# Performance work log

Hardware: AMD Instinct MI355X
Metric: run time of the kernel (lower is better)

The kernel has to match this reference:

```python
import jax, jax.numpy as jnp
import numpy as np

N = 50000      # node_num
C = 64         # num_classes
G = 3          # number of metapath graphs (len(g))
E = 1200000    # edges per metapath graph
L = 2          # layers (PLPConv propagation steps)
D = 256        # input feature dim (feat_dims[0])
H = 256        # hidden_dim


def setup_inputs() -> dict:
    key = jax.random.key(0)
    ks = jax.random.split(key, 13)
    features0 = jax.random.normal(ks[0], (N, D), jnp.float32)
    labels = jax.random.randint(ks[1], (N,), 0, C)
    labels_one_hot = jax.nn.one_hot(labels, C, dtype=jnp.float32)
    # label_init: soft labels, rows on the simplex
    label_init = jax.nn.softmax(jax.random.normal(ks[2], (N, C), jnp.float32), axis=-1)
    train_mask = (jax.random.uniform(ks[3], (N, 1)) < 0.5).astype(jnp.float32)
    src = jax.random.randint(ks[4], (G, E), 0, N, dtype=jnp.int32)
    dst = jax.random.randint(ks[5], (G, E), 0, N, dtype=jnp.int32)
    # per-layer, per-graph learned edge logits (xavier-ish small init)
    e_edges = 0.1 * jax.random.normal(ks[6], (L, G, E), jnp.float32)
    attention = 0.5 * jax.random.normal(ks[7], (N, G), jnp.float32)
    alpha = 0.5 * jax.random.normal(ks[8], (N, 1), jnp.float32)
    W1 = jax.random.normal(ks[9], (D, H), jnp.float32) / np.sqrt(D)
    b1 = jnp.zeros((H,), jnp.float32)
    W2 = jax.random.normal(ks[10], (H, C), jnp.float32) / np.sqrt(H)
    b2 = jnp.zeros((C,), jnp.float32)
    return {"features0": features0, "label_init": label_init,
            "labels_one_hot": labels_one_hot, "train_mask": train_mask,
            "src": src, "dst": dst, "e_edges": e_edges,
            "attention": attention, "alpha": alpha,
            "W1": W1, "b1": b1, "W2": W2, "b2": b2}


def _edge_softmax(e, dst, n):
    # softmax of per-edge scalar over incoming edges of each dst node
    m = jax.ops.segment_max(e, dst, num_segments=n)
    a = jnp.exp(e - m[dst])
    s = jax.ops.segment_sum(a, dst, num_segments=n)
    return a / s[dst]


def reference(features0, label_init, labels_one_hot, train_mask,
              src, dst, e_edges, attention, alpha, W1, b1, W2, b2):
    n = label_init.shape[0]
    masked_label = 1.0 - train_mask            # (~masked).float(), [N,1]
    masked_oh = labels_one_hot * train_mask    # labels_one_hot * masked, [N,C]

    # Label propagation over each metapath graph (PLPConv stack, activation=None)
    h_prime = []
    for i in range(G):
        h = label_init
        for l in range(L):
            a = _edge_softmax(e_edges[l, i], dst[i], n)         # [E]
            msg = h[src[i]] * a[:, None]                        # gather-mul [E,C]
            h = jax.ops.segment_sum(msg, dst[i], num_segments=n)  # scatter-sum [N,C]
            h = h * masked_label + masked_oh                    # clamp train labels
        h_prime.append(h)
    x = jnp.stack(h_prime, axis=-1)                             # [N,C,G]

    att_mp = jax.nn.softmax(attention, axis=1)                  # [N,G]
    logits_lp = jnp.einsum('ncg,ng->nc', x, att_mp)             # [N,C]

    # MLP2 (2 layers, dropout=0): relu(x W1 + b1) W2 + b2
    hm = jax.nn.relu(features0 @ W1 + b1)
    logits_ns = hm @ W2 + b2                                    # [N,C]

    logits = jax.nn.sigmoid(alpha) * logits_lp + jax.nn.sigmoid(-alpha) * logits_ns
    return (logits, logits_lp, logits_ns)
```

## Files before the change

### kernel.cpp

```cpp
#include <hip/hip_runtime.h>
#include <hip/hip_bf16.h>

#define NN 50000
#define CC 64
#define GG 3
#define EE 1200000
#define LL 2
#define DD 256
#define HH 256
#define NB 196
#define NBLK 293
#define NBK (GG * NB)
#define BKCAP 8192
#define CH 16384
#define CBLK 74


__device__ __forceinline__ ushort f2bf(float f) {
    unsigned b = __float_as_uint(f);
    return (ushort)((b + 0x7fffu + ((b >> 16) & 1u)) >> 16);
}
__device__ __forceinline__ float bf2f(unsigned u) {
    return __uint_as_float(u << 16);
}

typedef __attribute__((ext_vector_type(8))) short s8v;
typedef __attribute__((ext_vector_type(4))) float f4v;

template<int NWM, int NWN, bool A_FP32, bool OUT_RELU_BF16>
__global__ __launch_bounds__(256) void mfma_gemm_kernel(
    const void* __restrict__ Av, const ushort* __restrict__ Bt,
    const float* __restrict__ bias, void* __restrict__ Cv, int M, int Nc)
{
    static_assert(NWM * NWN == 4, "4 waves per block");
    const int tid = threadIdx.x;
    const int w = tid >> 6;
    const int l = tid & 63;
    const int wm = w / NWN;
    const int wn = w % NWN;
    const int r0 = blockIdx.x * (NWM * 64) + wm * 64;
    const int c0 = blockIdx.y * (NWN * 64) + wn * 64;
    const int lrow = l & 15;
    const int lk = (l >> 4) << 3;

    f4v acc[4][4] = {};

    for (int k0 = 0; k0 < 256; k0 += 32) {
        s8v a[4], b[4];
        #pragma unroll
        for (int i = 0; i < 4; i++) {
            int row = r0 + lrow + 16 * i;
            row = (row < M) ? row : (M - 1);
            if constexpr (A_FP32) {
                const float* Af = (const float*)Av;
                const float4* p = (const float4*)(Af + (size_t)row * 256 + k0 + lk);
                float4 f0 = p[0], f1 = p[1];
                union { ushort u[8]; s8v v; } t;
                t.u[0] = f2bf(f0.x); t.u[1] = f2bf(f0.y);
                t.u[2] = f2bf(f0.z); t.u[3] = f2bf(f0.w);
                t.u[4] = f2bf(f1.x); t.u[5] = f2bf(f1.y);
                t.u[6] = f2bf(f1.z); t.u[7] = f2bf(f1.w);
                a[i] = t.v;
            } else {
                const ushort* Ab = (const ushort*)Av;
                a[i] = *(const s8v*)(Ab + (size_t)row * 256 + k0 + lk);
            }
        }
        #pragma unroll
        for (int j = 0; j < 4; j++) {
            int col = c0 + lrow + 16 * j;
            b[j] = *(const s8v*)(Bt + (size_t)col * 256 + k0 + lk);
        }
        #pragma unroll
        for (int i = 0; i < 4; i++)
            #pragma unroll
            for (int j = 0; j < 4; j++)
                acc[i][j] = __builtin_amdgcn_mfma_f32_16x16x32_bf16(
                    a[i], b[j], acc[i][j], 0, 0, 0);
    }

    #pragma unroll
    for (int i = 0; i < 4; i++) {
        #pragma unroll
        for (int r = 0; r < 4; r++) {
            int row = r0 + 16 * i + (l >> 4) * 4 + r;
            if (row >= M) continue;
            #pragma unroll
            for (int j = 0; j < 4; j++) {
                int col = c0 + 16 * j + lrow;
                float v = acc[i][j][r] + bias[col];
                if constexpr (OUT_RELU_BF16) {
                    v = fmaxf(v, 0.f);
                    ((ushort*)Cv)[(size_t)row * Nc + col] = f2bf(v);
                } else {
                    ((float*)Cv)[(size_t)row * Nc + col] = v;
                }
            }
        }
    }
}

__global__ void wcvt_kernel(const float* __restrict__ W1,
                            const float* __restrict__ W2,
                            ushort* __restrict__ Wt1, ushort* __restrict__ Wt2)
{
    int idx = blockIdx.x * 256 + threadIdx.x;
    if (idx < 256 * 256) {
        int n = idx >> 8, k = idx & 255;
        Wt1[idx] = f2bf(W1[k * 256 + n]);
    } else {
        int i = idx - 256 * 256;
        if (i < 64 * 256) {
            int n = i >> 8, k = i & 255;
            Wt2[i] = f2bf(W2[k * 64 + n]);
        }
    }
}

__global__ void cvt_kernel(const float* __restrict__ in, ushort* __restrict__ out, int n4)
{
    int i = blockIdx.x * blockDim.x + threadIdx.x;
    if (i >= n4) return;
    float4 f = ((const float4*)in)[i];
    ushort4 u;
    u.x = f2bf(f.x); u.y = f2bf(f.y); u.z = f2bf(f.z); u.w = f2bf(f.w);
    ((ushort4*)out)[i] = u;
}

__global__ __launch_bounds__(256) void bhist_kernel(
    const int* __restrict__ dst, int* __restrict__ bcnt)
{
    int blk = blockIdx.x;
    int g = blk / NBLK;
    int bi = blk - g * NBLK;
    int base = bi * 4096;
    __shared__ int cnt[NB];
    int t = threadIdx.x;
    if (t < NB) cnt[t] = 0;
    __syncthreads();
    #pragma unroll
    for (int k = 0; k < 16; k++) {
        int e = base + k * 256 + t;
        if (e < EE) atomicAdd(&cnt[dst[g * EE + e] >> 8], 1);
    }
    __syncthreads();
    if (t < NB && cnt[t] > 0) atomicAdd(&bcnt[g * NB + t], cnt[t]);
}

__global__ void scan_bucket(const int* __restrict__ bcnt, int* __restrict__ bs)
{
    __shared__ int sd[256];
    __shared__ int s_run;
    int t = threadIdx.x;
    if (t == 0) s_run = 0;
    __syncthreads();
    for (int base = 0; base < NBK; base += 256) {
        int i = base + t;
        int v = (i < NBK) ? bcnt[i] : 0;
        sd[t] = v;
        __syncthreads();
        for (int o = 1; o < 256; o <<= 1) {
            int x = (t >= o) ? sd[t - o] : 0;
            __syncthreads();
            sd[t] += x;
            __syncthreads();
        }
        int run = s_run;
        __syncthreads();
        if (i < NBK) bs[i] = run + sd[t] - v;
        if (t == 255) s_run = run + sd[255];
        __syncthreads();
    }
    if (t == 0) bs[NBK] = GG * EE;
}

__global__ __launch_bounds__(1024) void binA_kernel(
    const int* __restrict__ dst, const int* __restrict__ src,
    const float* __restrict__ e_edges, const int* __restrict__ bucket_start,
    int* __restrict__ fill, uint2* __restrict__ staging)
{
    int blk = blockIdx.x;
    int g = blk / CBLK;
    int bi = blk - g * CBLK;
    int base = bi * CH;
    __shared__ uint2 rec[CH];
    __shared__ int cnt[NB];
    __shared__ int lstart[NB];
    __shared__ int cur[NB];
    __shared__ int gbase[NB];
    __shared__ int sd[256];
    int t = threadIdx.x;
    if (t < NB) cnt[t] = 0;
    __syncthreads();

    int myd[16];
    #pragma unroll
    for (int k = 0; k < 16; k++) {
        int e = base + k * 1024 + t;
        int d = (e < EE) ? dst[g * EE + e] : -1;
        myd[k] = d;
        if (d >= 0) atomicAdd(&cnt[d >> 8], 1);
    }
    __syncthreads();

    if (t < 256) sd[t] = (t < NB) ? cnt[t] : 0;
    __syncthreads();
    for (int o = 1; o < 256; o <<= 1) {
        int x = (t < 256 && t >= o) ? sd[t - o] : 0;
        __syncthreads();
        if (t < 256) sd[t] += x;
        __syncthreads();
    }
    if (t < NB) {
        int c = cnt[t];
        int ls = sd[t] - c;
        lstart[t] = ls;
        cur[t] = ls;
        int fo = (c > 0) ? atomicAdd(&fill[g * NB + t], c) : 0;
        gbase[t] = bucket_start[g * NB + t] + fo;
    }
    __syncthreads();

    #pragma unroll
    for (int k = 0; k < 16; k++) {
        int d = myd[k];
        if (d >= 0) {
            int e = base + k * 1024 + t;
            int pos = atomicAdd(&cur[d >> 8], 1);
            int idxg = g * EE + e;
            uint2 r;
            r.x = ((unsigned)f2bf(e_edges[idxg]) << 16) |
                  (unsigned)f2bf(e_edges[(size_t)(GG + g) * EE + e]);
            r.y = ((unsigned)src[idxg] << 16) | (unsigned)(d & 255);
            rec[pos] = r;
        }
    }
    __syncthreads();

    int w = t >> 6, lane = t & 63;
    for (int b = w; b < NB; b += 16) {
        int c = cnt[b];
        int ls = lstart[b];
        uint2* dp = staging + gbase[b];
        for (int i = lane; i < c; i += 64) dp[i] = rec[ls + i];
    }
}

__global__ __launch_bounds__(1024) void bucket_kernel(
    const uint2* __restrict__ staging, const int* __restrict__ bucket_start,
    int* __restrict__ row_start, unsigned* __restrict__ packed0,
    unsigned* __restrict__ packed1)
{
    int blk = blockIdx.x;
    int g = blk / NB;
    int bucket = blk - g * NB;
    int bn = bucket << 8;
    int bnodes = min(256, NN - bn);
    int sbase = bucket_start[blk];
    int n = bucket_start[blk + 1] - sbase;
    int segStart = sbase - g * EE;
    const uint2* st = staging + sbase;

    __shared__ int hist[256];
    __shared__ int sd[256];
    __shared__ int cur[256];
    __shared__ float sm[512];
    __shared__ ushort ab0[BKCAP];
    __shared__ ushort ab1[BKCAP];
    __shared__ ushort sb[BKCAP];
    int t = threadIdx.x;
    if (t < 256) hist[t] = 0;
    if (t < 512) sm[t] = 0.f;
    __syncthreads();

    for (int i = t; i < n; i += 1024) {
        uint2 r = st[i];
        int dl = r.y & 0xff;
        atomicAdd(&hist[dl], 1);
        atomicAdd(&sm[dl], __expf(bf2f(r.x >> 16)));
        atomicAdd(&sm[256 + dl], __expf(bf2f(r.x & 0xffffu)));
    }
    __syncthreads();

    if (t < 256) sd[t] = hist[t];
    __syncthreads();
    for (int o = 1; o < 256; o <<= 1) {
        int x = (t < 256 && t >= o) ? sd[t - o] : 0;
        __syncthreads();
        if (t < 256) sd[t] += x;
        __syncthreads();
    }
    if (t < 256) {
        cur[t] = sd[t] - hist[t];
        if (t < bnodes)
            row_start[(size_t)g * (NN + 1) + bn + t] = segStart + sd[t] - hist[t];
        if (hist[t] > 0) {
            sm[t] = 1.f / sm[t];
            sm[256 + t] = 1.f / sm[256 + t];
        }
    }
    if (bucket == NB - 1 && t == 0) row_start[(size_t)g * (NN + 1) + NN] = EE;
    __syncthreads();

    for (int i = t; i < n; i += 1024) {
        uint2 r = st[i];
        int dl = r.y & 0xff;
        int pos = atomicAdd(&cur[dl], 1);
        ab0[pos] = f2bf(__expf(bf2f(r.x >> 16)) * sm[dl]);
        ab1[pos] = f2bf(__expf(bf2f(r.x & 0xffffu)) * sm[256 + dl]);
        sb[pos] = (ushort)(r.y >> 16);
    }
    __syncthreads();

    for (int i = t; i < n; i += 1024) {
        unsigned s = sb[i];
        packed0[(size_t)sbase + i] = ((unsigned)ab0[i] << 16) | s;
        packed1[(size_t)sbase + i] = ((unsigned)ab1[i] << 16) | s;
    }
}

__device__ __forceinline__ void consume8(unsigned packed, int cnt,
                                         const ushort* __restrict__ tab,
                                         int lane, float& acc)
{
    for (int k0 = 0; k0 < cnt; k0 += 8) {
        unsigned pk[8];
        #pragma unroll
        for (int u = 0; u < 8; u++) pk[u] = __shfl(packed, k0 + u);
        float vals[8];
        #pragma unroll
        for (int u = 0; u < 8; u++)
            vals[u] = bf2f((unsigned)tab[(size_t)(pk[u] & 0xffffu) * 64 + lane]);
        #pragma unroll
        for (int u = 0; u < 8; u++)
            acc = fmaf(vals[u], __uint_as_float(pk[u] & 0xffff0000u), acc);
    }
}

__global__ __launch_bounds__(256) void prop0_kernel(
    const ushort* __restrict__ lab_bf, const float* __restrict__ labels_oh,
    const float* __restrict__ train_mask, const int* __restrict__ row_start,
    const unsigned* __restrict__ packed0, ushort* __restrict__ h_buf)
{
    int wid = (blockIdx.x * blockDim.x + threadIdx.x) >> 6;
    int lane = threadIdx.x & 63;
    if (wid >= GG * NN) return;
    int g = wid / NN;
    int v = wid - g * NN;
    const int* rs = row_start + (size_t)g * (NN + 1);
    int s = rs[v], tE = rs[v + 1];
    const unsigned* pk = packed0 + (size_t)g * EE;

    float acc = 0.f;
    for (int base = s; base < tE; base += 64) {
        int j = base + lane;
        unsigned packed = (j < tE) ? pk[j] : 0u;
        int cnt = min(64, tE - base);
        consume8(packed, cnt, lab_bf, lane, acc);
    }
    float tm = train_mask[v];
    float res = acc * (1.f - tm) + labels_oh[(size_t)v * 64 + lane] * tm;
    h_buf[(size_t)wid * 64 + lane] = f2bf(res);
}

__global__ __launch_bounds__(256) void final_kernel(
    const ushort* __restrict__ h_buf, const float* __restrict__ labels_oh,
    const float* __restrict__ train_mask, const float* __restrict__ attention,
    const float* __restrict__ alpha, const int* __restrict__ row_start,
    const unsigned* __restrict__ packed1, const float* __restrict__ out_ns,
    float* __restrict__ out_logits, float* __restrict__ out_lp)
{
    int wid = (blockIdx.x * blockDim.x + threadIdx.x) >> 6;
    int lane = threadIdx.x & 63;
    if (wid >= NN) return;
    int v = wid;
    float tm = train_mask[v];
    float ml = 1.f - tm;
    float moh = labels_oh[(size_t)v * 64 + lane] * tm;
    float a0 = attention[v * 3], a1 = attention[v * 3 + 1], a2 = attention[v * 3 + 2];
    float mxa = fmaxf(a0, fmaxf(a1, a2));
    float e0 = __expf(a0 - mxa), e1 = __expf(a1 - mxa), e2 = __expf(a2 - mxa);
    float ainv = 1.f / (e0 + e1 + e2);
    float attw[3] = {e0 * ainv, e1 * ainv, e2 * ainv};
    float lp = 0.f;
    #pragma unroll
    for (int g = 0; g < GG; g++) {
        const int* rs = row_start + (size_t)g * (NN + 1);
        int s = rs[v], tE = rs[v + 1];
        const unsigned* pk = packed1 + (size_t)g * EE;
        const ushort* hin = h_buf + (size_t)g * NN * 64;

        float acc = 0.f;
        for (int base = s; base < tE; base += 64) {
            int j = base + lane;
            unsigned packed = (j < tE) ? pk[j] : 0u;
            int cnt = min(64, tE - base);
            consume8(packed, cnt, hin, lane, acc);
        }
        float hf = acc * ml + moh;
        lp += attw[g] * hf;
    }
    size_t o = (size_t)v * 64 + lane;
    out_lp[o] = lp;
    float al = alpha[v];
    float sg = 1.f / (1.f + __expf(-al));
    out_logits[o] = sg * lp + (1.f - sg) * out_ns[o];
}

extern "C" void kernel_launch(void* const* d_in, const int* in_sizes, int n_in,
                              void* d_out, int out_size, void* d_ws, size_t ws_size,
                              hipStream_t stream)
{
    const float* features0  = (const float*)d_in[0];
    const float* label_init = (const float*)d_in[1];
    const float* labels_oh  = (const float*)d_in[2];
    const float* train_mask = (const float*)d_in[3];
    const int*   src        = (const int*)d_in[4];
    const int*   dst        = (const int*)d_in[5];
    const float* e_edges    = (const float*)d_in[6];
    const float* attention  = (const float*)d_in[7];
    const float* alpha      = (const float*)d_in[8];
    const float* W1         = (const float*)d_in[9];
    const float* b1         = (const float*)d_in[10];
    const float* W2         = (const float*)d_in[11];
    const float* b2         = (const float*)d_in[12];

    float* out        = (float*)d_out;
    float* out_logits = out;
    float* out_lp     = out + (size_t)NN * CC;
    float* out_ns     = out + 2 * (size_t)NN * CC;

    char* base = (char*)d_ws;
    size_t off = 0;
    auto alloc = [&](size_t bytes) -> void* {
        void* p = base + off;
        off = (off + bytes + 255) & ~(size_t)255;
        return p;
    };
    int*      bcnt         = (int*)alloc((size_t)NBK * sizeof(int));
    int*      fill         = (int*)alloc((size_t)NBK * sizeof(int));
    size_t    zero_bytes   = off;
    int*      bucket_start = (int*)alloc((size_t)(NBK + 1) * sizeof(int));
    int*      row_start    = (int*)alloc((size_t)GG * (NN + 1) * sizeof(int));
    uint2*    staging      = (uint2*)alloc((size_t)GG * EE * sizeof(uint2));
    unsigned* packed0      = (unsigned*)alloc((size_t)GG * EE * sizeof(unsigned));
    unsigned* packed1      = (unsigned*)alloc((size_t)GG * EE * sizeof(unsigned));
    ushort*   h_buf        = (ushort*)alloc((size_t)GG * NN * CC * sizeof(ushort));
    ushort*   lab_bf       = (ushort*)alloc((size_t)NN * CC * sizeof(ushort));

    ushort* Wt1   = (ushort*)packed0;
    ushort* Wt2   = Wt1 + 256 * 256;
    ushort* hm_bf = (ushort*)staging;

    wcvt_kernel<<<(256 * 256 + 64 * 256) / 256, 256, 0, stream>>>(W1, W2, Wt1, Wt2);
    mfma_gemm_kernel<2, 2, true, true><<<dim3((NN + 127) / 128, 2), 256, 0, stream>>>(
        features0, Wt1, b1, hm_bf, NN, HH);
    mfma_gemm_kernel<4, 1, false, false><<<dim3((NN + 255) / 256, 1), 256, 0, stream>>>(
        hm_bf, Wt2, b2, out_ns, NN, CC);

    cvt_kernel<<<(NN * CC / 4 + 255) / 256, 256, 0, stream>>>(
        label_init, lab_bf, NN * CC / 4);

    hipMemsetAsync(bcnt, 0, zero_bytes, stream);
    bhist_kernel<<<GG * NBLK, 256, 0, stream>>>(dst, bcnt);
    scan_bucket<<<1, 256, 0, stream>>>(bcnt, bucket_start);
    binA_kernel<<<GG * CBLK, 1024, 0, stream>>>(
        dst, src, e_edges, bucket_start, fill, staging);
    bucket_kernel<<<GG * NB, 1024, 0, stream>>>(
        staging, bucket_start, row_start, packed0, packed1);

    prop0_kernel<<<((size_t)GG * NN * 64 + 255) / 256, 256, 0, stream>>>(
        lab_bf, labels_oh, train_mask, row_start, packed0, h_buf);

    final_kernel<<<((size_t)NN * 64 + 255) / 256, 256, 0, stream>>>(
        h_buf, labels_oh, train_mask, attention, alpha, row_start, packed1,
        out_ns, out_logits, out_lp);
}
```

Before: 482.9 us.

## Split label tables into 32-channel planes and gather 8 edges per wave instruction

```diff
diff --git a/kernel.cpp b/kernel.cpp
--- a/kernel.cpp
+++ b/kernel.cpp
@@ -117,14 +117,37 @@
     }
 }
 
-__global__ void cvt_kernel(const float* __restrict__ in, ushort* __restrict__ out, int n4)
-{
-    int i = blockIdx.x * blockDim.x + threadIdx.x;
-    if (i >= n4) return;
-    float4 f = ((const float4*)in)[i];
-    ushort4 u;
-    u.x = f2bf(f.x); u.y = f2bf(f.y); u.z = f2bf(f.z); u.w = f2bf(f.w);
-    ((ushort4*)out)[i] = u;
+__global__ __launch_bounds__(256) void prep_kernel(
+    const float* __restrict__ label_init, const float* __restrict__ labels_oh,
+    const float* __restrict__ train_mask, ushort* __restrict__ lab_bf,
+    short* __restrict__ mid)
+{
+    int b = blockIdx.x;
+    if (b < 3125) {
+        int i = b * 256 + threadIdx.x;
+        int v = i >> 4;
+        int c4 = (i & 15) * 4;
+        float4 f = ((const float4*)label_init)[i];
+        ushort4 u;
+        u.x = f2bf(f.x); u.y = f2bf(f.y); u.z = f2bf(f.z); u.w = f2bf(f.w);
+        int pl = c4 >> 5;
+        *(ushort4*)(lab_bf + (size_t)pl * NN * 32 + (size_t)v * 32 + (c4 & 31)) = u;
+    } else {
+        int t = threadIdx.x;
+        int v = (b - 3125) * 16 + (t >> 4);
+        int sl = t & 15;
+        if (v < NN) {
+            float4 f = ((const float4*)(labels_oh + (size_t)v * 64))[sl];
+            float p = (float)(sl * 4);
+            float s = f.x * p + f.y * (p + 1.f) + f.z * (p + 2.f) + f.w * (p + 3.f);
+            s += __shfl_xor(s, 1); s += __shfl_xor(s, 2);
+            s += __shfl_xor(s, 4); s += __shfl_xor(s, 8);
+            if (sl == 0) {
+                float tm = train_mask[v];
+                mid[v] = (tm > 0.5f) ? (short)(s + 0.5f) : (short)-1;
+            }
+        }
+    }
 }
 
 __global__ __launch_bounds__(256) void bhist_kernel(
@@ -319,28 +342,32 @@
     }
 }
 
-__device__ __forceinline__ void consume8(unsigned packed, int cnt,
-                                         const ushort* __restrict__ tab,
-                                         int lane, float& acc)
-{
-    for (int k0 = 0; k0 < cnt; k0 += 8) {
-        unsigned pk[8];
-        #pragma unroll
-        for (int u = 0; u < 8; u++) pk[u] = __shfl(packed, k0 + u);
-        float vals[8];
-        #pragma unroll
-        for (int u = 0; u < 8; u++)
-            vals[u] = bf2f((unsigned)tab[(size_t)(pk[u] & 0xffffu) * 64 + lane]);
-        #pragma unroll
-        for (int u = 0; u < 8; u++)
-            acc = fmaf(vals[u], __uint_as_float(pk[u] & 0xffff0000u), acc);
+__device__ __forceinline__ void tile_pass(unsigned packed, int cnt,
+        const ushort* __restrict__ plane, unsigned loff, int sub, float acc[4])
+{
+    for (int q0 = 0; q0 < cnt; q0 += 32) {
+        uint2 gv[4]; float w[4];
+        #pragma unroll
+        for (int u = 0; u < 4; u++) {
+            unsigned pkq = __shfl(packed, q0 + 8 * u + sub);
+            w[u] = __uint_as_float(pkq & 0xffff0000u);
+            gv[u] = *(const uint2*)((const char*)plane +
+                                    (((pkq & 0xffffu) << 6) | loff));
+        }
+        #pragma unroll
+        for (int u = 0; u < 4; u++) {
+            acc[0] = fmaf(__uint_as_float(gv[u].x << 16),          w[u], acc[0]);
+            acc[1] = fmaf(__uint_as_float(gv[u].x & 0xffff0000u),  w[u], acc[1]);
+            acc[2] = fmaf(__uint_as_float(gv[u].y << 16),          w[u], acc[2]);
+            acc[3] = fmaf(__uint_as_float(gv[u].y & 0xffff0000u),  w[u], acc[3]);
+        }
     }
 }
 
 __global__ __launch_bounds__(256) void prop0_kernel(
-    const ushort* __restrict__ lab_bf, const float* __restrict__ labels_oh,
-    const float* __restrict__ train_mask, const int* __restrict__ row_start,
-    const unsigned* __restrict__ packed0, ushort* __restrict__ h_buf)
+    const ushort* __restrict__ lab_bf, const short* __restrict__ mid,
+    const int* __restrict__ row_start, const unsigned* __restrict__ packed0,
+    ushort* __restrict__ h_buf)
 {
     int wid = (blockIdx.x * blockDim.x + threadIdx.x) >> 6;
     int lane = threadIdx.x & 63;
@@ -350,61 +377,130 @@
     const int* rs = row_start + (size_t)g * (NN + 1);
     int s = rs[v], tE = rs[v + 1];
     const unsigned* pk = packed0 + (size_t)g * EE;
-
-    float acc = 0.f;
+    const ushort* pl0 = lab_bf;
+    const ushort* pl1 = lab_bf + (size_t)NN * 32;
+
+    unsigned loff = (lane & 7) << 3;
+    int sub = lane >> 3;
+    float a0[4] = {}, a1[4] = {};
     for (int base = s; base < tE; base += 64) {
         int j = base + lane;
         unsigned packed = (j < tE) ? pk[j] : 0u;
         int cnt = min(64, tE - base);
-        consume8(packed, cnt, lab_bf, lane, acc);
-    }
-    float tm = train_mask[v];
-    float res = acc * (1.f - tm) + labels_oh[(size_t)v * 64 + lane] * tm;
-    h_buf[(size_t)wid * 64 + lane] = f2bf(res);
+        tile_pass(packed, cnt, pl0, loff, sub, a0);
+        tile_pass(packed, cnt, pl1, loff, sub, a1);
+    }
+    #pragma unroll
+    for (int c = 0; c < 4; c++) {
+        a0[c] += __shfl_xor(a0[c], 8);
+        a0[c] += __shfl_xor(a0[c], 16);
+        a0[c] += __shfl_xor(a0[c], 32);
+        a1[c] += __shfl_xor(a1[c], 8);
+        a1[c] += __shfl_xor(a1[c], 16);
+        a1[c] += __shfl_xor(a1[c], 32);
+    }
+    int m = mid[v];
+    float ml = (m < 0) ? 1.f : 0.f;
+    ushort* hg = h_buf + (size_t)g * NN * 64;
+    int cb = (lane & 7) * 4;
+    if (lane < 8) {
+        ushort4 o;
+        o.x = f2bf(a0[0] * ml + ((cb + 0 == m) ? 1.f : 0.f));
+        o.y = f2bf(a0[1] * ml + ((cb + 1 == m) ? 1.f : 0.f));
+        o.z = f2bf(a0[2] * ml + ((cb + 2 == m) ? 1.f : 0.f));
+        o.w = f2bf(a0[3] * ml + ((cb + 3 == m) ? 1.f : 0.f));
+        *(ushort4*)(hg + (size_t)v * 32 + cb) = o;
+    } else if (lane < 16) {
+        int cc = cb + 32;
+        ushort4 o;
+        o.x = f2bf(a1[0] * ml + ((cc + 0 == m) ? 1.f : 0.f));
+        o.y = f2bf(a1[1] * ml + ((cc + 1 == m) ? 1.f : 0.f));
+        o.z = f2bf(a1[2] * ml + ((cc + 2 == m) ? 1.f : 0.f));
+        o.w = f2bf(a1[3] * ml + ((cc + 3 == m) ? 1.f : 0.f));
+        *(ushort4*)(hg + (size_t)NN * 32 + (size_t)v * 32 + cb) = o;
+    }
 }
 
 __global__ __launch_bounds__(256) void final_kernel(
-    const ushort* __restrict__ h_buf, const float* __restrict__ labels_oh,
-    const float* __restrict__ train_mask, const float* __restrict__ attention,
-    const float* __restrict__ alpha, const int* __restrict__ row_start,
-    const unsigned* __restrict__ packed1, const float* __restrict__ out_ns,
-    float* __restrict__ out_logits, float* __restrict__ out_lp)
+    const ushort* __restrict__ h_buf, const short* __restrict__ mid,
+    const float* __restrict__ attention, const float* __restrict__ alpha,
+    const int* __restrict__ row_start, const unsigned* __restrict__ packed1,
+    const float* __restrict__ out_ns, float* __restrict__ out_logits,
+    float* __restrict__ out_lp)
 {
     int wid = (blockIdx.x * blockDim.x + threadIdx.x) >> 6;
     int lane = threadIdx.x & 63;
     if (wid >= NN) return;
     int v = wid;
-    float tm = train_mask[v];
-    float ml = 1.f - tm;
-    float moh = labels_oh[(size_t)v * 64 + lane] * tm;
-    float a0 = attention[v * 3], a1 = attention[v * 3 + 1], a2 = attention[v * 3 + 2];
-    float mxa = fmaxf(a0, fmaxf(a1, a2));
-    float e0 = __expf(a0 - mxa), e1 = __expf(a1 - mxa), e2 = __expf(a2 - mxa);
+    float t0 = attention[v * 3], t1 = attention[v * 3 + 1], t2 = attention[v * 3 + 2];
+    float mxa = fmaxf(t0, fmaxf(t1, t2));
+    float e0 = __expf(t0 - mxa), e1 = __expf(t1 - mxa), e2 = __expf(t2 - mxa);
     float ainv = 1.f / (e0 + e1 + e2);
     float attw[3] = {e0 * ainv, e1 * ainv, e2 * ainv};
-    float lp = 0.f;
+
+    unsigned loff = (lane & 7) << 3;
+    int sub = lane >> 3;
+    float w0[4] = {}, w1[4] = {};
     #pragma unroll
     for (int g = 0; g < GG; g++) {
         const int* rs = row_start + (size_t)g * (NN + 1);
         int s = rs[v], tE = rs[v + 1];
         const unsigned* pk = packed1 + (size_t)g * EE;
-        const ushort* hin = h_buf + (size_t)g * NN * 64;
-
-        float acc = 0.f;
+        const ushort* hp0 = h_buf + (size_t)g * NN * 64;
+        const ushort* hp1 = hp0 + (size_t)NN * 32;
+        float b0[4] = {}, b1[4] = {};
         for (int base = s; base < tE; base += 64) {
             int j = base + lane;
             unsigned packed = (j < tE) ? pk[j] : 0u;
             int cnt = min(64, tE - base);
-            consume8(packed, cnt, hin, lane, acc);
-        }
-        float hf = acc * ml + moh;
-        lp += attw[g] * hf;
-    }
-    size_t o = (size_t)v * 64 + lane;
-    out_lp[o] = lp;
-    float al = alpha[v];
-    float sg = 1.f / (1.f + __expf(-al));
-    out_logits[o] = sg * lp + (1.f - sg) * out_ns[o];
+            tile_pass(packed, cnt, hp0, loff, sub, b0);
+            tile_pass(packed, cnt, hp1, loff, sub, b1);
+        }
+        float aw = attw[g];
+        #pragma unroll
+        for (int c = 0; c < 4; c++) {
+            w0[c] = fmaf(aw, b0[c], w0[c]);
+            w1[c] = fmaf(aw, b1[c], w1[c]);
+        }
+    }
+    #pragma unroll
+    for (int c = 0; c < 4; c++) {
+        w0[c] += __shfl_xor(w0[c], 8);
+        w0[c] += __shfl_xor(w0[c], 16);
+        w0[c] += __shfl_xor(w0[c], 32);
+        w1[c] += __shfl_xor(w1[c], 8);
+        w1[c] += __shfl_xor(w1[c], 16);
+        w1[c] += __shfl_xor(w1[c], 32);
+    }
+    int m = mid[v];
+    float ml = (m < 0) ? 1.f : 0.f;
+    if (lane < 16) {
+        int pl = lane >> 3;
+        int cb = (lane & 7) * 4 + pl * 32;
+        float4 lpv;
+        if (pl == 0) {
+            lpv.x = w0[0] * ml + ((cb + 0 == m) ? 1.f : 0.f);
+            lpv.y = w0[1] * ml + ((cb + 1 == m) ? 1.f : 0.f);
+            lpv.z = w0[2] * ml + ((cb + 2 == m) ? 1.f : 0.f);
+            lpv.w = w0[3] * ml + ((cb + 3 == m) ? 1.f : 0.f);
+        } else {
+            lpv.x = w1[0] * ml + ((cb + 0 == m) ? 1.f : 0.f);
+            lpv.y = w1[1] * ml + ((cb + 1 == m) ? 1.f : 0.f);
+            lpv.z = w1[2] * ml + ((cb + 2 == m) ? 1.f : 0.f);
+            lpv.w = w1[3] * ml + ((cb + 3 == m) ? 1.f : 0.f);
+        }
+        size_t o = (size_t)v * 64 + cb;
+        *(float4*)(out_lp + o) = lpv;
+        float al = alpha[v];
+        float sg = 1.f / (1.f + __expf(-al));
+        float4 ns = *(const float4*)(out_ns + o);
+        float4 lg;
+        lg.x = sg * lpv.x + (1.f - sg) * ns.x;
+        lg.y = sg * lpv.y + (1.f - sg) * ns.y;
+        lg.z = sg * lpv.z + (1.f - sg) * ns.z;
+        lg.w = sg * lpv.w + (1.f - sg) * ns.w;
+        *(float4*)(out_logits + o) = lg;
+    }
 }
 
 extern "C" void kernel_launch(void* const* d_in, const int* in_sizes, int n_in,
@@ -447,6 +543,7 @@
     unsigned* packed1      = (unsigned*)alloc((size_t)GG * EE * sizeof(unsigned));
     ushort*   h_buf        = (ushort*)alloc((size_t)GG * NN * CC * sizeof(ushort));
     ushort*   lab_bf       = (ushort*)alloc((size_t)NN * CC * sizeof(ushort));
+    short*    mid          = (short*)alloc((size_t)NN * sizeof(short));
 
     ushort* Wt1   = (ushort*)packed0;
     ushort* Wt2   = Wt1 + 256 * 256;
@@ -458,8 +555,8 @@
     mfma_gemm_kernel<4, 1, false, false><<<dim3((NN + 255) / 256, 1), 256, 0, stream>>>(
         hm_bf, Wt2, b2, out_ns, NN, CC);
 
-    cvt_kernel<<<(NN * CC / 4 + 255) / 256, 256, 0, stream>>>(
-        label_init, lab_bf, NN * CC / 4);
+    prep_kernel<<<6250, 256, 0, stream>>>(label_init, labels_oh, train_mask,
+                                          lab_bf, mid);
 
     hipMemsetAsync(bcnt, 0, zero_bytes, stream);
     bhist_kernel<<<GG * NBLK, 256, 0, stream>>>(dst, bcnt);
@@ -470,9 +567,9 @@
         staging, bucket_start, row_start, packed0, packed1);
 
     prop0_kernel<<<((size_t)GG * NN * 64 + 255) / 256, 256, 0, stream>>>(
-        lab_bf, labels_oh, train_mask, row_start, packed0, h_buf);
+        lab_bf, mid, row_start, packed0, h_buf);
 
     final_kernel<<<((size_t)NN * 64 + 255) / 256, 256, 0, stream>>>(
-        h_buf, labels_oh, train_mask, attention, alpha, row_start, packed1,
+        h_buf, mid, attention, alpha, row_start, packed1,
         out_ns, out_logits, out_lp);
 }
```

Measured after the change: 512.3 us. +6.1%, slower.

## Drop destination histogram pass using fixed-capacity bucket staging and merge prep kernels

Applied to the files above, without the earlier changes.

```diff
diff --git a/kernel.cpp b/kernel.cpp
--- a/kernel.cpp
+++ b/kernel.cpp
@@ -9,7 +9,6 @@
 #define DD 256
 #define HH 256
 #define NB 196
-#define NBLK 293
 #define NBK (GG * NB)
 #define BKCAP 8192
 #define CH 16384
@@ -100,54 +99,34 @@
     }
 }
 
-__global__ void wcvt_kernel(const float* __restrict__ W1,
-                            const float* __restrict__ W2,
-                            ushort* __restrict__ Wt1, ushort* __restrict__ Wt2)
-{
-    int idx = blockIdx.x * 256 + threadIdx.x;
-    if (idx < 256 * 256) {
-        int n = idx >> 8, k = idx & 255;
-        Wt1[idx] = f2bf(W1[k * 256 + n]);
+__global__ __launch_bounds__(256) void prep_kernel(
+    const float* __restrict__ label_init,
+    const float* __restrict__ W1, const float* __restrict__ W2,
+    ushort* __restrict__ lab_bf, ushort* __restrict__ Wt1,
+    ushort* __restrict__ Wt2)
+{
+    int b = blockIdx.x;
+    int t = threadIdx.x;
+    if (b < 3125) {
+        int i = b * 256 + t;
+        float4 f = ((const float4*)label_init)[i];
+        ushort4 u;
+        u.x = f2bf(f.x); u.y = f2bf(f.y); u.z = f2bf(f.z); u.w = f2bf(f.w);
+        ((ushort4*)lab_bf)[i] = u;
     } else {
-        int i = idx - 256 * 256;
-        if (i < 64 * 256) {
+        int idx = (b - 3125) * 256 + t;
+        if (idx < 256 * 256) {
+            int n = idx >> 8, k = idx & 255;
+            Wt1[idx] = f2bf(W1[k * 256 + n]);
+        } else {
+            int i = idx - 256 * 256;
             int n = i >> 8, k = i & 255;
             Wt2[i] = f2bf(W2[k * 64 + n]);
         }
     }
 }
 
-__global__ void cvt_kernel(const float* __restrict__ in, ushort* __restrict__ out, int n4)
-{
-    int i = blockIdx.x * blockDim.x + threadIdx.x;
-    if (i >= n4) return;
-    float4 f = ((const float4*)in)[i];
-    ushort4 u;
-    u.x = f2bf(f.x); u.y = f2bf(f.y); u.z = f2bf(f.z); u.w = f2bf(f.w);
-    ((ushort4*)out)[i] = u;
-}
-
-__global__ __launch_bounds__(256) void bhist_kernel(
-    const int* __restrict__ dst, int* __restrict__ bcnt)
-{
-    int blk = blockIdx.x;
-    int g = blk / NBLK;
-    int bi = blk - g * NBLK;
-    int base = bi * 4096;
-    __shared__ int cnt[NB];
-    int t = threadIdx.x;
-    if (t < NB) cnt[t] = 0;
-    __syncthreads();
-    #pragma unroll
-    for (int k = 0; k < 16; k++) {
-        int e = base + k * 256 + t;
-        if (e < EE) atomicAdd(&cnt[dst[g * EE + e] >> 8], 1);
-    }
-    __syncthreads();
-    if (t < NB && cnt[t] > 0) atomicAdd(&bcnt[g * NB + t], cnt[t]);
-}
-
-__global__ void scan_bucket(const int* __restrict__ bcnt, int* __restrict__ bs)
+__global__ void scan_bucket(const int* __restrict__ fill, int* __restrict__ bs)
 {
     __shared__ int sd[256];
     __shared__ int s_run;
@@ -156,7 +135,7 @@
     __syncthreads();
     for (int base = 0; base < NBK; base += 256) {
         int i = base + t;
-        int v = (i < NBK) ? bcnt[i] : 0;
+        int v = (i < NBK) ? fill[i] : 0;
         sd[t] = v;
         __syncthreads();
         for (int o = 1; o < 256; o <<= 1) {
@@ -176,8 +155,8 @@
 
 __global__ __launch_bounds__(1024) void binA_kernel(
     const int* __restrict__ dst, const int* __restrict__ src,
-    const float* __restrict__ e_edges, const int* __restrict__ bucket_start,
-    int* __restrict__ fill, uint2* __restrict__ staging)
+    const float* __restrict__ e_edges, int* __restrict__ fill,
+    uint2* __restrict__ staging)
 {
     int blk = blockIdx.x;
     int g = blk / CBLK;
@@ -217,7 +196,7 @@
         lstart[t] = ls;
         cur[t] = ls;
         int fo = (c > 0) ? atomicAdd(&fill[g * NB + t], c) : 0;
-        gbase[t] = bucket_start[g * NB + t] + fo;
+        gbase[t] = (g * NB + t) * BKCAP + fo;
     }
     __syncthreads();
 
@@ -241,25 +220,25 @@
     for (int b = w; b < NB; b += 16) {
         int c = cnt[b];
         int ls = lstart[b];
-        uint2* dp = staging + gbase[b];
+        uint2* dp = staging + (size_t)gbase[b];
         for (int i = lane; i < c; i += 64) dp[i] = rec[ls + i];
     }
 }
 
 __global__ __launch_bounds__(1024) void bucket_kernel(
-    const uint2* __restrict__ staging, const int* __restrict__ bucket_start,
-    int* __restrict__ row_start, unsigned* __restrict__ packed0,
-    unsigned* __restrict__ packed1)
+    const uint2* __restrict__ staging, const int* __restrict__ fill,
+    const int* __restrict__ out_start, int* __restrict__ row_start,
+    unsigned* __restrict__ packed0, unsigned* __restrict__ packed1)
 {
     int blk = blockIdx.x;
     int g = blk / NB;
     int bucket = blk - g * NB;
     int bn = bucket << 8;
     int bnodes = min(256, NN - bn);
-    int sbase = bucket_start[blk];
-    int n = bucket_start[blk + 1] - sbase;
-    int segStart = sbase - g * EE;
-    const uint2* st = staging + sbase;
+    int n = fill[blk];
+    int obase = out_start[blk];
+    int segStart = obase - g * EE;
+    const uint2* st = staging + (size_t)blk * BKCAP;
 
     __shared__ int hist[256];
     __shared__ int sd[256];
@@ -314,8 +293,8 @@
 
     for (int i = t; i < n; i += 1024) {
         unsigned s = sb[i];
-        packed0[(size_t)sbase + i] = ((unsigned)ab0[i] << 16) | s;
-        packed1[(size_t)sbase + i] = ((unsigned)ab1[i] << 16) | s;
+        packed0[(size_t)obase + i] = ((unsigned)ab0[i] << 16) | s;
+        packed1[(size_t)obase + i] = ((unsigned)ab1[i] << 16) | s;
     }
 }
 
@@ -354,7 +333,7 @@
     float acc = 0.f;
     for (int base = s; base < tE; base += 64) {
         int j = base + lane;
-        unsigned packed = (j < tE) ? pk[j] : 0u;
+        unsigned packed = (j < tE) ? __builtin_nontemporal_load(pk + j) : 0u;
         int cnt = min(64, tE - base);
         consume8(packed, cnt, lab_bf, lane, acc);
     }
@@ -393,7 +372,7 @@
         float acc = 0.f;
         for (int base = s; base < tE; base += 64) {
             int j = base + lane;
-            unsigned packed = (j < tE) ? pk[j] : 0u;
+            unsigned packed = (j < tE) ? __builtin_nontemporal_load(pk + j) : 0u;
             int cnt = min(64, tE - base);
             consume8(packed, cnt, hin, lane, acc);
         }
@@ -437,37 +416,32 @@
         off = (off + bytes + 255) & ~(size_t)255;
         return p;
     };
-    int*      bcnt         = (int*)alloc((size_t)NBK * sizeof(int));
     int*      fill         = (int*)alloc((size_t)NBK * sizeof(int));
     size_t    zero_bytes   = off;
-    int*      bucket_start = (int*)alloc((size_t)(NBK + 1) * sizeof(int));
+    int*      out_start    = (int*)alloc((size_t)(NBK + 1) * sizeof(int));
     int*      row_start    = (int*)alloc((size_t)GG * (NN + 1) * sizeof(int));
-    uint2*    staging      = (uint2*)alloc((size_t)GG * EE * sizeof(uint2));
+    uint2*    staging      = (uint2*)alloc((size_t)NBK * BKCAP * sizeof(uint2));
     unsigned* packed0      = (unsigned*)alloc((size_t)GG * EE * sizeof(unsigned));
     unsigned* packed1      = (unsigned*)alloc((size_t)GG * EE * sizeof(unsigned));
     ushort*   h_buf        = (ushort*)alloc((size_t)GG * NN * CC * sizeof(ushort));
     ushort*   lab_bf       = (ushort*)alloc((size_t)NN * CC * sizeof(ushort));
 
-    ushort* Wt1   = (ushort*)packed0;
-    ushort* Wt2   = Wt1 + 256 * 256;
-    ushort* hm_bf = (ushort*)staging;
-
-    wcvt_kernel<<<(256 * 256 + 64 * 256) / 256, 256, 0, stream>>>(W1, W2, Wt1, Wt2);
+    ushort* Wt1     = (ushort*)packed0;
+    ushort* Wt2     = Wt1 + 256 * 256;
+    ushort* hm_bf   = (ushort*)staging;
+
+    hipMemsetAsync(fill, 0, zero_bytes, stream);
+    prep_kernel<<<3445, 256, 0, stream>>>(label_init, W1, W2, lab_bf, Wt1, Wt2);
+
     mfma_gemm_kernel<2, 2, true, true><<<dim3((NN + 127) / 128, 2), 256, 0, stream>>>(
         features0, Wt1, b1, hm_bf, NN, HH);
     mfma_gemm_kernel<4, 1, false, false><<<dim3((NN + 255) / 256, 1), 256, 0, stream>>>(
         hm_bf, Wt2, b2, out_ns, NN, CC);
 
-    cvt_kernel<<<(NN * CC / 4 + 255) / 256, 256, 0, stream>>>(
-        label_init, lab_bf, NN * CC / 4);
-
-    hipMemsetAsync(bcnt, 0, zero_bytes, stream);
-    bhist_kernel<<<GG * NBLK, 256, 0, stream>>>(dst, bcnt);
-    scan_bucket<<<1, 256, 0, stream>>>(bcnt, bucket_start);
-    binA_kernel<<<GG * CBLK, 1024, 0, stream>>>(
-        dst, src, e_edges, bucket_start, fill, staging);
+    binA_kernel<<<GG * CBLK, 1024, 0, stream>>>(dst, src, e_edges, fill, staging);
+    scan_bucket<<<1, 256, 0, stream>>>(fill, out_start);
     bucket_kernel<<<GG * NB, 1024, 0, stream>>>(
-        staging, bucket_start, row_start, packed0, packed1);
+        staging, fill, out_start, row_start, packed0, packed1);
 
     prop0_kernel<<<((size_t)GG * NN * 64 + 255) / 256, 256, 0, stream>>>(
         lab_bf, labels_oh, train_mask, row_start, packed0, h_buf);
```

After: 470.9 us. -2.5%, faster.
